# Kernel optimization log

Measured on AMD Instinct MI355X. Metric: run time of the kernel, lower is better.

The kernel has to match this reference:

```python
import jax, jax.numpy as jnp
import numpy as np
import math

N, B, S = 2048, 4, 1024
SFZ, IFZ, H, A = 384, 256, 8, 64
LN_EPS = 1e-5


def setup_inputs() -> dict:
    key = jax.random.key(0)
    ks = jax.random.split(key, 12)
    x = jax.random.normal(ks[0], (N, IFZ), dtype=jnp.float32)
    emb = jax.random.normal(ks[1], (B, S, SFZ), dtype=jnp.float32)
    mask = jax.random.randint(ks[2], (B, S), 0, 2).astype(bool)
    batch = jnp.sort(jax.random.randint(ks[3], (N,), 0, B)).astype(jnp.int64)
    sc = 1.0 / math.sqrt(IFZ)
    scs = 1.0 / math.sqrt(SFZ)
    Wq = jax.random.normal(ks[4], (IFZ, H * A), dtype=jnp.float32) * sc
    Wk = jax.random.normal(ks[5], (SFZ, H * A), dtype=jnp.float32) * scs
    Wv = jax.random.normal(ks[6], (SFZ, H * A), dtype=jnp.float32) * scs
    Wg = jax.random.normal(ks[7], (IFZ, H * A), dtype=jnp.float32) * sc
    bg = jnp.zeros((H * A,), dtype=jnp.float32)
    Wback = jax.random.normal(ks[8], (H * A, IFZ), dtype=jnp.float32) / math.sqrt(H * A)
    bback = jnp.zeros((IFZ,), dtype=jnp.float32)
    gamma = jnp.ones((IFZ,), dtype=jnp.float32)
    beta = jnp.zeros((IFZ,), dtype=jnp.float32)
    return {"x": x, "packed_sequence_emb": emb, "packed_sequence_mask": mask,
            "batch": batch, "Wq": Wq, "Wk": Wk, "Wv": Wv, "Wg": Wg, "bg": bg,
            "Wback": Wback, "bback": bback, "gamma": gamma, "beta": beta}


def _masked_softmax(scores, mask):
    # scores: [N,S,H], mask: [N,S,1] bool; softmax over S with padded entries zeroed
    neg = jnp.finfo(scores.dtype).min
    s = jnp.where(mask, scores, neg)
    s = s - jnp.max(s, axis=1, keepdims=True)
    e = jnp.exp(s) * mask
    return e / (jnp.sum(e, axis=1, keepdims=True) + 1e-9)


def reference(x, packed_sequence_emb, packed_sequence_mask, batch,
              Wq, Wk, Wv, Wg, bg, Wback, bback, gamma, beta):
    scale = math.sqrt(A)
    q = (x @ Wq).reshape(N, H, A)                               # [N,H,A]
    k = (packed_sequence_emb @ Wk).reshape(B, S, H, A)          # [B,S,H,A]
    v = (packed_sequence_emb @ Wv).reshape(B, S, H, A)
    # scores per (node, candidate-batch), then gather node's own batch entry;
    # avoids materializing k[batch] of shape [N,S,H,A]
    scores_all = jnp.einsum('nha,bsha->nbsh', q, k) / scale     # [N,B,S,H]
    idx = batch[:, None, None, None].astype(jnp.int32)
    scores = jnp.take_along_axis(scores_all, idx, axis=1)[:, 0]  # [N,S,H]
    bmask = packed_sequence_mask[batch][..., None]               # [N,S,1]
    w = _masked_softmax(scores, bmask)                           # [N,S,H]
    feat_all = jnp.einsum('nsh,bsha->nbha', w, v)                # [N,B,H,A]
    feat = jnp.take_along_axis(feat_all, idx, axis=1)[:, 0]      # [N,H,A]
    gate = jax.nn.sigmoid(x @ Wg + bg).reshape(N, H, A)
    new = (gate * feat).reshape(N, H * A) @ Wback + bback        # [N,IFZ]
    y = math.sqrt(2.0) * x + new
    mu = jnp.mean(y, axis=-1, keepdims=True)
    var = jnp.mean((y - mu) ** 2, axis=-1, keepdims=True)
    out = (y - mu) * jax.lax.rsqrt(var + LN_EPS) * gamma + beta
    seq_aa_logits = jnp.sum(scores[..., :2], axis=-1)            # [N,S]
    return out, seq_aa_logits
```

## Files before the change

kernel.cpp:

```cpp
#include <hip/hip_runtime.h>
#include <hip/hip_bf16.h>

#define NND 2048
#define BBATCH 4
#define SS 1024
#define SFZ 384
#define IFZ 256
#define HH 8
#define AA 64
#define HA 512
#define NBX 48
#define NSPL 8

typedef __attribute__((ext_vector_type(8))) short bf16x8;
typedef __attribute__((ext_vector_type(4))) float f32x4;

__device__ __forceinline__ unsigned short f2bf(float f) {
    union { float f; unsigned u; } a; a.f = f;
    unsigned r = a.u + 0x7fffu + ((a.u >> 16) & 1u);
    return (unsigned short)(r >> 16);
}
__device__ __forceinline__ float bf2f(unsigned short u) {
    return __uint_as_float((unsigned)u << 16);
}

__device__ __forceinline__ bf16x8 cvt8(const float* __restrict__ p) {
    const float4 f0 = *(const float4*)p;
    const float4 f1 = *(const float4*)(p + 4);
    bf16x8 o;
    o[0] = (short)f2bf(f0.x); o[1] = (short)f2bf(f0.y);
    o[2] = (short)f2bf(f0.z); o[3] = (short)f2bf(f0.w);
    o[4] = (short)f2bf(f1.x); o[5] = (short)f2bf(f1.y);
    o[6] = (short)f2bf(f1.z); o[7] = (short)f2bf(f1.w);
    return o;
}

__device__ __forceinline__ void tile_transpose(
    const float* __restrict__ src, unsigned short* __restrict__ dst,
    int K, int N, int kt, int nt, int t)
{
    __shared__ unsigned short tile[64][65];
    const int k0 = kt * 64, n0 = nt * 64;
    const int tr = t >> 6, tc = t & 63;
    #pragma unroll
    for (int r = 0; r < 16; ++r)
        tile[tr + r*4][tc] = f2bf(src[(size_t)(k0 + tr + r*4) * N + n0 + tc]);
    __syncthreads();
    #pragma unroll
    for (int r = 0; r < 16; ++r)
        dst[(size_t)(n0 + tr + r*4) * K + k0 + tc] = tile[tc][tr + r*4];
}

__global__ __launch_bounds__(256) void prep_kernel(
    const float* __restrict__ Wk, const float* __restrict__ Wv,
    const float* __restrict__ Wq, const float* __restrict__ Wg,
    const float* __restrict__ Wback,
    const void* __restrict__ mask_raw, const void* __restrict__ batch_raw,
    unsigned short* __restrict__ WkT, unsigned short* __restrict__ WvT,
    unsigned short* __restrict__ WqT, unsigned short* __restrict__ WgT,
    unsigned short* __restrict__ WbackT,
    float* __restrict__ mask_f, int* __restrict__ seg)
{
    const int bx = blockIdx.x, t = threadIdx.x;
    if (bx < 48)  { tile_transpose(Wk, WkT, SFZ, HA, bx/8, bx%8, t); return; }
    if (bx < 96)  { const int i = bx-48;  tile_transpose(Wv, WvT, SFZ, HA, i/8, i%8, t); return; }
    if (bx < 128) { const int i = bx-96;  tile_transpose(Wq, WqT, IFZ, HA, i/8, i%8, t); return; }
    if (bx < 160) { const int i = bx-128; tile_transpose(Wg, WgT, IFZ, HA, i/8, i%8, t); return; }
    if (bx < 192) { const int i = bx-160; tile_transpose(Wback, WbackT, HA, IFZ, i/4, i%4, t); return; }
    __shared__ int fl[4];
    __shared__ int fb;
    __shared__ int cnt[4];
    if (t < 4) { fl[t] = 0; cnt[t] = 0; }
    if (t == 0) fb = 0;
    __syncthreads();
    const unsigned char*  mb = (const unsigned char*)mask_raw;
    const unsigned short* mh = (const unsigned short*)mask_raw;
    const unsigned int*   mw = (const unsigned int*)mask_raw;
    int f0 = 0, f1 = 0, f2 = 0, f3 = 0;
    for (int i = t; i < 2048; i += 256) {
        unsigned short h = mh[i];
        if (h == 0x3f80u) f0 = 1;
        if ((i & 1) == 0 && h != 0) f1 = 1;
    }
    for (int i = t; i < 4096; i += 256)
        if ((i & 3) != 0 && mb[i] != 0) f2 = 1;
    for (int i = t; i < 1024; i += 256)
        if ((i & 1) != 0 && mw[i] != 0) f3 = 1;
    const int* bw = (const int*)batch_raw;
    int f4 = 0;
    for (int i = t + 1; i < 2048; i += 256)
        if (bw[i] < bw[i-1]) f4 = 1;
    if (f0) atomicOr(&fl[0], 1);
    if (f1) atomicOr(&fl[1], 1);
    if (f2) atomicOr(&fl[2], 1);
    if (f3) atomicOr(&fl[3], 1);
    if (f4) atomicOr(&fb, 1);
    __syncthreads();
    int mode;
    if (fl[0])      mode = fl[1] ? 1 : 0;
    else if (fl[2]) mode = 2;
    else if (fl[3]) mode = 3;
    else            mode = 4;
    for (int s = t; s < BBATCH*SS; s += 256) {
        int m;
        switch (mode) {
            case 0:  m = (mw[s]   != 0); break;
            case 1:  m = (mh[s]   != 0); break;
            case 2:  m = (mb[s]   != 0); break;
            case 3:  m = (mw[s]   != 0); break;
            default: m = (mw[2*s] != 0); break;
        }
        mask_f[s] = m ? 1.0f : 0.0f;
    }
    const int b64 = fb;
    for (int i = t; i < NND; i += 256) {
        const int bv = (b64 ? bw[2*i] : bw[i]) & 3;
        atomicAdd(&cnt[bv], 1);
    }
    __syncthreads();
    if (t == 0) {
        int s = 0;
        for (int b = 0; b < 4; ++b) { seg[2*b] = s; s += cnt[b]; seg[2*b+1] = s; }
    }
}

__global__ __launch_bounds__(256) void proj_mfma(
    const float* __restrict__ emb, const float* __restrict__ x,
    const unsigned short* __restrict__ WkT, const unsigned short* __restrict__ WvT,
    const unsigned short* __restrict__ WqT, const unsigned short* __restrict__ WgT,
    const float* __restrict__ bg,
    unsigned short* __restrict__ k_blk, unsigned short* __restrict__ vT_bf,
    unsigned short* __restrict__ q_bf, float* __restrict__ gate_ws)
{
    __shared__ unsigned short v_l[16][520];
    const int t = threadIdx.x, w = t >> 6, lane = t & 63;
    const int m16 = lane & 15, quad = lane >> 4;
    const int bx = blockIdx.x;
    if (bx < 512) {
        const int r0 = (bx >> 1) * 16;
        const int b = r0 >> 10, srow = r0 & (SS - 1);
        const float* ap = emb + (size_t)(r0 + m16) * SFZ + quad * 8;
        bf16x8 af[12];
        #pragma unroll
        for (int j = 0; j < 12; ++j) af[j] = cvt8(ap + j * 32);
        if ((bx & 1) == 0) {
            #pragma unroll
            for (int nt = 0; nt < 8; ++nt) {
                const int n0 = w * 128 + nt * 16;
                const unsigned short* bp = WkT + (size_t)(n0 + m16) * SFZ + quad * 8;
                f32x4 d = (f32x4){0.f, 0.f, 0.f, 0.f};
                #pragma unroll
                for (int j = 0; j < 12; ++j)
                    d = __builtin_amdgcn_mfma_f32_16x16x32_bf16(af[j], *(const bf16x8*)(bp + j * 32), d, 0, 0, 0);
                const int head = n0 >> 6, coff = (n0 & 63) + m16;
                unsigned short* kb = k_blk + (((size_t)(b * HH + head)) * SS) * 64 + coff;
                #pragma unroll
                for (int r = 0; r < 4; ++r)
                    kb[(size_t)(srow + quad * 4 + r) * 64] = f2bf(d[r]);
            }
        } else {
            #pragma unroll
            for (int nt = 0; nt < 8; ++nt) {
                const int n0 = w * 128 + nt * 16;
                const unsigned short* bp = WvT + (size_t)(n0 + m16) * SFZ + quad * 8;
                f32x4 d = (f32x4){0.f, 0.f, 0.f, 0.f};
                #pragma unroll
                for (int j = 0; j < 12; ++j)
                    d = __builtin_amdgcn_mfma_f32_16x16x32_bf16(af[j], *(const bf16x8*)(bp + j * 32), d, 0, 0, 0);
                #pragma unroll
                for (int r = 0; r < 4; ++r)
                    v_l[quad * 4 + r][n0 + m16] = f2bf(d[r]);
            }
            __syncthreads();
            for (int c = t; c < HA; c += 256) {
                unsigned short tmp[16];
                #pragma unroll
                for (int s = 0; s < 16; ++s) tmp[s] = v_l[s][c];
                unsigned short* dst = vT_bf + ((size_t)b * HA + c) * SS + srow;
                *(uint4*)dst       = ((const uint4*)tmp)[0];
                *(uint4*)(dst + 8) = ((const uint4*)tmp)[1];
            }
        }
    } else {
        const int i = bx - 512;
        const int r0 = (i >> 2) * 16;
        const int tensor = (i & 3) >> 1, half = i & 1;
        const unsigned short* Wt = tensor ? WgT : WqT;
        const float* ap = x + (size_t)(r0 + m16) * IFZ + quad * 8;
        bf16x8 af[8];
        #pragma unroll
        for (int j = 0; j < 8; ++j) af[j] = cvt8(ap + j * 32);
        #pragma unroll
        for (int nt = 0; nt < 4; ++nt) {
            const int n0 = half * 256 + w * 64 + nt * 16;
            const unsigned short* bp = Wt + (size_t)(n0 + m16) * IFZ + quad * 8;
            f32x4 d = (f32x4){0.f, 0.f, 0.f, 0.f};
            #pragma unroll
            for (int j = 0; j < 8; ++j)
                d = __builtin_amdgcn_mfma_f32_16x16x32_bf16(af[j], *(const bf16x8*)(bp + j * 32), d, 0, 0, 0);
            if (tensor == 0) {
                #pragma unroll
                for (int r = 0; r < 4; ++r)
                    q_bf[(size_t)(r0 + quad * 4 + r) * HA + n0 + m16] = f2bf(d[r]);
            } else {
                const float bgv = bg[n0 + m16];
                #pragma unroll
                for (int r = 0; r < 4; ++r)
                    gate_ws[(size_t)(r0 + quad * 4 + r) * HA + n0 + m16] =
                        1.f / (1.f + __expf(-(d[r] + bgv)));
            }
        }
    }
}

__global__ __launch_bounds__(256) void attn_kernel(
    const unsigned short* __restrict__ k_blk, const unsigned short* __restrict__ vT_bf,
    const unsigned short* __restrict__ q_bf, const float* __restrict__ mask_f,
    const int* __restrict__ seg, unsigned short* __restrict__ part_O,
    float2* __restrict__ part_ml, float* __restrict__ out_logits)
{
    __shared__ unsigned short P_lds[4][16][136];
    __shared__ float raw[2][16][132];
    const int bid = blockIdx.x;
    const int xcd = bid & 7;
    const int b   = xcd >> 1;
    const int idx = (bid >> 3) * 2 + (xcd & 1);
    const int z    = idx & 15;
    const int xblk = idx >> 4;
    const int hz    = z >> 3;
    const int split = z & 7;
    const int n0 = seg[2*b] + xblk * 16;
    const int nend = seg[2*b + 1];
    if (n0 >= nend) return;
    const int nvalid = min(16, nend - n0);

    const int t = threadIdx.x;
    const int w = t >> 6, lane = t & 63;
    const int m16 = lane & 15, quad = lane >> 4;
    const int h = hz * 4 + w;
    const int s0 = split * 128;

    int nq = n0 + m16; if (nq >= nend) nq = nend - 1;
    const unsigned short* qp = q_bf + (size_t)nq * HA + h * AA + quad * 8;
    const bf16x8 qa0 = *(const bf16x8*)qp;
    const bf16x8 qa1 = *(const bf16x8*)(qp + 32);

    const unsigned short* kb = k_blk + ((size_t)(b * HH + h)) * SS * 64;
    const unsigned short* vb = vT_bf + ((size_t)b * HA + h * AA) * SS;
    unsigned short (*Pw)[136] = P_lds[w];

    float msk[8];
    #pragma unroll
    for (int st = 0; st < 8; ++st)
        msk[st] = mask_f[b * SS + s0 + st * 16 + m16];

    f32x4 d[8];
    #pragma unroll
    for (int st = 0; st < 8; ++st) {
        const unsigned short* kp = kb + (size_t)(s0 + st * 16 + m16) * 64 + quad * 8;
        const bf16x8 b0 = *(const bf16x8*)kp;
        const bf16x8 b1 = *(const bf16x8*)(kp + 32);
        f32x4 acc = (f32x4){0.f, 0.f, 0.f, 0.f};
        acc = __builtin_amdgcn_mfma_f32_16x16x32_bf16(qa0, b0, acc, 0, 0, 0);
        acc = __builtin_amdgcn_mfma_f32_16x16x32_bf16(qa1, b1, acc, 0, 0, 0);
        #pragma unroll
        for (int r = 0; r < 4; ++r) acc[r] *= 0.125f;
        d[st] = acc;
    }
    if (hz == 0) {
        if (w < 2) {
            #pragma unroll
            for (int st = 0; st < 8; ++st)
                #pragma unroll
                for (int r = 0; r < 4; ++r)
                    raw[w][quad * 4 + r][st * 16 + m16] = d[st][r];
        }
        __syncthreads();
        for (int i = t; i < 16 * 128; i += 256) {
            const int node = i >> 7, sp = i & 127;
            if (node < nvalid)
                out_logits[(size_t)(n0 + node) * SS + s0 + sp] =
                    raw[0][node][sp] + raw[1][node][sp];
        }
    }
    float m_s[4], l_s[4];
    #pragma unroll
    for (int r = 0; r < 4; ++r) {
        float mx = -3.0e38f;
        #pragma unroll
        for (int st = 0; st < 8; ++st)
            mx = (msk[st] > 0.5f) ? fmaxf(mx, d[st][r]) : mx;
        mx = fmaxf(mx, __shfl_xor(mx, 1));
        mx = fmaxf(mx, __shfl_xor(mx, 2));
        mx = fmaxf(mx, __shfl_xor(mx, 4));
        mx = fmaxf(mx, __shfl_xor(mx, 8));
        m_s[r] = mx;
        float cs = 0.f;
        #pragma unroll
        for (int st = 0; st < 8; ++st) {
            const float e = (msk[st] > 0.5f) ? __expf(d[st][r] - mx) : 0.f;
            d[st][r] = e;
            cs += e;
        }
        cs += __shfl_xor(cs, 1);
        cs += __shfl_xor(cs, 2);
        cs += __shfl_xor(cs, 4);
        cs += __shfl_xor(cs, 8);
        l_s[r] = cs;
    }
    #pragma unroll
    for (int st = 0; st < 8; ++st)
        #pragma unroll
        for (int r = 0; r < 4; ++r)
            Pw[quad * 4 + r][st * 16 + m16] = f2bf(d[st][r]);
    f32x4 facc[4];
    #pragma unroll
    for (int a = 0; a < 4; ++a) facc[a] = (f32x4){0.f, 0.f, 0.f, 0.f};
    #pragma unroll
    for (int sub = 0; sub < 4; ++sub) {
        const bf16x8 pa = *(const bf16x8*)&Pw[m16][sub * 32 + quad * 8];
        const unsigned short* vp0 = vb + (size_t)m16 * SS + s0 + sub * 32 + quad * 8;
        #pragma unroll
        for (int a = 0; a < 4; ++a) {
            const bf16x8 vfr = *(const bf16x8*)(vp0 + (size_t)(a * 16) * SS);
            facc[a] = __builtin_amdgcn_mfma_f32_16x16x32_bf16(pa, vfr, facc[a], 0, 0, 0);
        }
    }
    unsigned short* po = part_O + (size_t)split * NND * HA;
    #pragma unroll
    for (int a = 0; a < 4; ++a)
        #pragma unroll
        for (int r = 0; r < 4; ++r) {
            const int row = quad * 4 + r;
            if (row < nvalid)
                po[(size_t)(n0 + row) * HA + h * AA + a * 16 + m16] = f2bf(facc[a][r]);
        }
    if (m16 == 0) {
        #pragma unroll
        for (int r = 0; r < 4; ++r) {
            const int row = quad * 4 + r;
            if (row < nvalid)
                part_ml[(size_t)split * NND * HH + (size_t)(n0 + row) * HH + h] =
                    make_float2(m_s[r], l_s[r]);
        }
    }
}

__global__ __launch_bounds__(256) void back_ln_fused(
    const unsigned short* __restrict__ part_O, const float2* __restrict__ part_ml,
    const float* __restrict__ gate_ws, const unsigned short* __restrict__ WbackT,
    const float* __restrict__ x, const float* __restrict__ bback,
    const float* __restrict__ gamma, const float* __restrict__ beta,
    float* __restrict__ out)
{
    __shared__ float coef[NSPL][8][8];
    __shared__ unsigned short gf_l[8][520];
    __shared__ float nl[8][260];
    const int t = threadIdx.x, w = t >> 6, lane = t & 63;
    const int m16 = lane & 15, quad = lane >> 4;
    const int r0 = blockIdx.x * 8;
    if (t < 64) {
        const int row = t >> 3, h = t & 7, n = r0 + row;
        float2 ml[NSPL];
        #pragma unroll
        for (int s = 0; s < NSPL; ++s)
            ml[s] = part_ml[(size_t)s * NND * HH + (size_t)n * HH + h];
        float M = -3.0e38f;
        #pragma unroll
        for (int s = 0; s < NSPL; ++s) M = fmaxf(M, ml[s].x);
        float L = 0.f;
        float e[NSPL];
        #pragma unroll
        for (int s = 0; s < NSPL; ++s) { e[s] = __expf(ml[s].x - M); L += ml[s].y * e[s]; }
        const float invL = 1.f / (L + 1e-9f);
        #pragma unroll
        for (int s = 0; s < NSPL; ++s) coef[s][row][h] = e[s] * invL;
    }
    __syncthreads();
    #pragma unroll
    for (int it = 0; it < 4; ++it) {
        const int i = (t + it * 256) * 4;
        const int row = i >> 9, c = i & (HA - 1), h = c >> 6;
        const int n = r0 + row;
        float4 o = make_float4(0.f, 0.f, 0.f, 0.f);
        #pragma unroll
        for (int s = 0; s < NSPL; ++s) {
            const ushort4 p = *(const ushort4*)&part_O[(size_t)s * NND * HA + (size_t)n * HA + c];
            const float cf = coef[s][row][h];
            o.x = fmaf(bf2f(p.x), cf, o.x); o.y = fmaf(bf2f(p.y), cf, o.y);
            o.z = fmaf(bf2f(p.z), cf, o.z); o.w = fmaf(bf2f(p.w), cf, o.w);
        }
        const float4 g = *(const float4*)&gate_ws[(size_t)n * HA + c];
        ushort4 ob;
        ob.x = f2bf(g.x * o.x); ob.y = f2bf(g.y * o.y);
        ob.z = f2bf(g.z * o.z); ob.w = f2bf(g.w * o.w);
        *(ushort4*)&gf_l[row][c] = ob;
    }
    __syncthreads();
    bf16x8 af[16];
    #pragma unroll
    for (int j = 0; j < 16; ++j)
        af[j] = *(const bf16x8*)&gf_l[m16 & 7][quad * 8 + j * 32];
    #pragma unroll
    for (int nt = 0; nt < 4; ++nt) {
        const int n0 = w * 64 + nt * 16;
        const unsigned short* bp = WbackT + (size_t)(n0 + m16) * HA + quad * 8;
        f32x4 d = (f32x4){0.f, 0.f, 0.f, 0.f};
        #pragma unroll
        for (int j = 0; j < 16; ++j)
            d = __builtin_amdgcn_mfma_f32_16x16x32_bf16(af[j], *(const bf16x8*)(bp + j * 32), d, 0, 0, 0);
        const float bb = bback[n0 + m16];
        #pragma unroll
        for (int r = 0; r < 4; ++r) {
            const int rr = quad * 4 + r;
            if (rr < 8) nl[rr][n0 + m16] = d[r] + bb;
        }
    }
    __syncthreads();
    const int row = t >> 5, li = t & 31;
    const float* xr = x + (size_t)(r0 + row) * IFZ;
    float yv[8];
    float s1 = 0.f, s2 = 0.f;
    #pragma unroll
    for (int j = 0; j < 8; ++j) {
        const int c = li + j * 32;
        const float v = fmaf(1.41421356237309515f, xr[c], nl[row][c]);
        yv[j] = v; s1 += v; s2 += v * v;
    }
    #pragma unroll
    for (int off = 16; off >= 1; off >>= 1) {
        s1 += __shfl_xor(s1, off);
        s2 += __shfl_xor(s2, off);
    }
    const float mu  = s1 * (1.f / IFZ);
    const float var = s2 * (1.f / IFZ) - mu * mu;
    const float rv  = rsqrtf(var + 1e-5f);
    float* orow = out + (size_t)(r0 + row) * IFZ;
    #pragma unroll
    for (int j = 0; j < 8; ++j) {
        const int c = li + j * 32;
        orow[c] = (yv[j] - mu) * rv * gamma[c] + beta[c];
    }
}

extern "C" void kernel_launch(void* const* d_in, const int* in_sizes, int n_in,
                              void* d_out, int out_size, void* d_ws, size_t ws_size,
                              hipStream_t stream) {
    const float* x     = (const float*)d_in[0];
    const float* emb   = (const float*)d_in[1];
    const void*  mraw  = d_in[2];
    const void*  braw  = d_in[3];
    const float* Wq    = (const float*)d_in[4];
    const float* Wk    = (const float*)d_in[5];
    const float* Wv    = (const float*)d_in[6];
    const float* Wg    = (const float*)d_in[7];
    const float* bg    = (const float*)d_in[8];
    const float* Wback = (const float*)d_in[9];
    const float* bback = (const float*)d_in[10];
    const float* gamma = (const float*)d_in[11];
    const float* beta  = (const float*)d_in[12];

    char* ws = (char*)d_ws;
    const size_t MB = 1048576;
    size_t off = 0;
    float*          mask_f  = (float*)(ws + off);  off += 16384;
    int*            seg     = (int*)(ws + off);    off += 16384;
    unsigned short* WkT     = (unsigned short*)(ws + off); off += 393216;
    unsigned short* WvT     = (unsigned short*)(ws + off); off += 393216;
    unsigned short* WqT     = (unsigned short*)(ws + off); off += 262144;
    unsigned short* WgT     = (unsigned short*)(ws + off); off += 262144;
    unsigned short* WbackT  = (unsigned short*)(ws + off); off += 262144;
    unsigned short* k_blk   = (unsigned short*)(ws + off); off += 4*MB;
    unsigned short* vT_bf   = (unsigned short*)(ws + off); off += 4*MB;
    unsigned short* q_bf    = (unsigned short*)(ws + off); off += 2*MB;
    float*          gate_ws = (float*)(ws + off); off += 4*MB;
    unsigned short* part_O  = (unsigned short*)(ws + off); off += 16*MB;
    float2*         part_ml = (float2*)(ws + off); off += 1*MB;

    float* out        = (float*)d_out;
    float* out_logits = out + (size_t)NND * IFZ;

    hipLaunchKernelGGL(prep_kernel, dim3(193), dim3(256), 0, stream,
                       Wk, Wv, Wq, Wg, Wback, mraw, braw,
                       WkT, WvT, WqT, WgT, WbackT, mask_f, seg);
    hipLaunchKernelGGL(proj_mfma, dim3(1024), dim3(256), 0, stream,
                       emb, x, WkT, WvT, WqT, WgT, bg, k_blk, vT_bf, q_bf, gate_ws);
    hipLaunchKernelGGL(attn_kernel, dim3(BBATCH * NBX * 16), dim3(256), 0, stream,
                       k_blk, vT_bf, q_bf, mask_f, seg, part_O, part_ml, out_logits);
    hipLaunchKernelGGL(back_ln_fused, dim3(NND / 8), dim3(256), 0, stream,
                       part_O, part_ml, gate_ws, WbackT, x, bback, gamma, beta, out);
}
```

Before: 198.5 us.

## Split weight transposes, store gate in bf16, halve rows per back-proj block

Each weight-transpose tile is split across two blocks, doubling the prep grid so more CUs take part. The sigmoid gate is now stored as bf16 instead of fp32, halving its write and read traffic between the projection and back-projection kernels. The fused back-projection/LayerNorm kernel now handles 4 rows per block instead of 8, doubling the grid for better occupancy, though half of each MFMA tile's rows go unused and WbackT is re-read by more blocks.

```diff
diff --git a/kernel.cpp b/kernel.cpp
--- a/kernel.cpp
+++ b/kernel.cpp
@@ -35,20 +35,21 @@
     return o;
 }
 
-__device__ __forceinline__ void tile_transpose(
+__device__ __forceinline__ void tile_transpose_h(
     const float* __restrict__ src, unsigned short* __restrict__ dst,
-    int K, int N, int kt, int nt, int t)
+    int K, int N, int kt, int nt, int half, int t)
 {
-    __shared__ unsigned short tile[64][65];
-    const int k0 = kt * 64, n0 = nt * 64;
+    __shared__ unsigned short tile[32][65];
+    const int k0 = kt * 64 + half * 32, n0 = nt * 64;
     const int tr = t >> 6, tc = t & 63;
     #pragma unroll
-    for (int r = 0; r < 16; ++r)
+    for (int r = 0; r < 8; ++r)
         tile[tr + r*4][tc] = f2bf(src[(size_t)(k0 + tr + r*4) * N + n0 + tc]);
     __syncthreads();
-    #pragma unroll
-    for (int r = 0; r < 16; ++r)
-        dst[(size_t)(n0 + tr + r*4) * K + k0 + tc] = tile[tc][tr + r*4];
+    const int rr = t >> 5, cc = t & 31;
+    #pragma unroll
+    for (int r2 = 0; r2 < 8; ++r2)
+        dst[(size_t)(n0 + rr + r2*8) * K + k0 + cc] = tile[cc][rr + r2*8];
 }
 
 __global__ __launch_bounds__(256) void prep_kernel(
@@ -62,11 +63,15 @@
     float* __restrict__ mask_f, int* __restrict__ seg)
 {
     const int bx = blockIdx.x, t = threadIdx.x;
-    if (bx < 48)  { tile_transpose(Wk, WkT, SFZ, HA, bx/8, bx%8, t); return; }
-    if (bx < 96)  { const int i = bx-48;  tile_transpose(Wv, WvT, SFZ, HA, i/8, i%8, t); return; }
-    if (bx < 128) { const int i = bx-96;  tile_transpose(Wq, WqT, IFZ, HA, i/8, i%8, t); return; }
-    if (bx < 160) { const int i = bx-128; tile_transpose(Wg, WgT, IFZ, HA, i/8, i%8, t); return; }
-    if (bx < 192) { const int i = bx-160; tile_transpose(Wback, WbackT, HA, IFZ, i/4, i%4, t); return; }
+    if (bx < 384) {
+        const int ht = bx >> 1, half = bx & 1;
+        if (ht < 48)       tile_transpose_h(Wk, WkT, SFZ, HA, ht/8, ht%8, half, t);
+        else if (ht < 96)  { const int i = ht-48;  tile_transpose_h(Wv, WvT, SFZ, HA, i/8, i%8, half, t); }
+        else if (ht < 128) { const int i = ht-96;  tile_transpose_h(Wq, WqT, IFZ, HA, i/8, i%8, half, t); }
+        else if (ht < 160) { const int i = ht-128; tile_transpose_h(Wg, WgT, IFZ, HA, i/8, i%8, half, t); }
+        else               { const int i = ht-160; tile_transpose_h(Wback, WbackT, HA, IFZ, i/4, i%4, half, t); }
+        return;
+    }
     __shared__ int fl[4];
     __shared__ int fb;
     __shared__ int cnt[4];
@@ -130,7 +135,7 @@
     const unsigned short* __restrict__ WqT, const unsigned short* __restrict__ WgT,
     const float* __restrict__ bg,
     unsigned short* __restrict__ k_blk, unsigned short* __restrict__ vT_bf,
-    unsigned short* __restrict__ q_bf, float* __restrict__ gate_ws)
+    unsigned short* __restrict__ q_bf, unsigned short* __restrict__ gate_bf)
 {
     __shared__ unsigned short v_l[16][520];
     const int t = threadIdx.x, w = t >> 6, lane = t & 63;
@@ -206,8 +211,8 @@
                 const float bgv = bg[n0 + m16];
                 #pragma unroll
                 for (int r = 0; r < 4; ++r)
-                    gate_ws[(size_t)(r0 + quad * 4 + r) * HA + n0 + m16] =
-                        1.f / (1.f + __expf(-(d[r] + bgv)));
+                    gate_bf[(size_t)(r0 + quad * 4 + r) * HA + n0 + m16] =
+                        f2bf(1.f / (1.f + __expf(-(d[r] + bgv))));
             }
         }
     }
@@ -348,18 +353,18 @@
 
 __global__ __launch_bounds__(256) void back_ln_fused(
     const unsigned short* __restrict__ part_O, const float2* __restrict__ part_ml,
-    const float* __restrict__ gate_ws, const unsigned short* __restrict__ WbackT,
+    const unsigned short* __restrict__ gate_bf, const unsigned short* __restrict__ WbackT,
     const float* __restrict__ x, const float* __restrict__ bback,
     const float* __restrict__ gamma, const float* __restrict__ beta,
     float* __restrict__ out)
 {
-    __shared__ float coef[NSPL][8][8];
-    __shared__ unsigned short gf_l[8][520];
-    __shared__ float nl[8][260];
+    __shared__ float coef[NSPL][4][8];
+    __shared__ unsigned short gf_l[4][520];
+    __shared__ float nl[4][260];
     const int t = threadIdx.x, w = t >> 6, lane = t & 63;
     const int m16 = lane & 15, quad = lane >> 4;
-    const int r0 = blockIdx.x * 8;
-    if (t < 64) {
+    const int r0 = blockIdx.x * 4;
+    if (t < 32) {
         const int row = t >> 3, h = t & 7, n = r0 + row;
         float2 ml[NSPL];
         #pragma unroll
@@ -378,7 +383,7 @@
     }
     __syncthreads();
     #pragma unroll
-    for (int it = 0; it < 4; ++it) {
+    for (int it = 0; it < 2; ++it) {
         const int i = (t + it * 256) * 4;
         const int row = i >> 9, c = i & (HA - 1), h = c >> 6;
         const int n = r0 + row;
@@ -390,17 +395,17 @@
             o.x = fmaf(bf2f(p.x), cf, o.x); o.y = fmaf(bf2f(p.y), cf, o.y);
             o.z = fmaf(bf2f(p.z), cf, o.z); o.w = fmaf(bf2f(p.w), cf, o.w);
         }
-        const float4 g = *(const float4*)&gate_ws[(size_t)n * HA + c];
+        const ushort4 g = *(const ushort4*)&gate_bf[(size_t)n * HA + c];
         ushort4 ob;
-        ob.x = f2bf(g.x * o.x); ob.y = f2bf(g.y * o.y);
-        ob.z = f2bf(g.z * o.z); ob.w = f2bf(g.w * o.w);
+        ob.x = f2bf(bf2f(g.x) * o.x); ob.y = f2bf(bf2f(g.y) * o.y);
+        ob.z = f2bf(bf2f(g.z) * o.z); ob.w = f2bf(bf2f(g.w) * o.w);
         *(ushort4*)&gf_l[row][c] = ob;
     }
     __syncthreads();
     bf16x8 af[16];
     #pragma unroll
     for (int j = 0; j < 16; ++j)
-        af[j] = *(const bf16x8*)&gf_l[m16 & 7][quad * 8 + j * 32];
+        af[j] = *(const bf16x8*)&gf_l[m16 & 3][quad * 8 + j * 32];
     #pragma unroll
     for (int nt = 0; nt < 4; ++nt) {
         const int n0 = w * 64 + nt * 16;
@@ -413,22 +418,22 @@
         #pragma unroll
         for (int r = 0; r < 4; ++r) {
             const int rr = quad * 4 + r;
-            if (rr < 8) nl[rr][n0 + m16] = d[r] + bb;
-        }
-    }
-    __syncthreads();
-    const int row = t >> 5, li = t & 31;
+            if (rr < 4) nl[rr][n0 + m16] = d[r] + bb;
+        }
+    }
+    __syncthreads();
+    const int row = t >> 6, li = t & 63;
     const float* xr = x + (size_t)(r0 + row) * IFZ;
-    float yv[8];
+    float yv[4];
     float s1 = 0.f, s2 = 0.f;
     #pragma unroll
-    for (int j = 0; j < 8; ++j) {
-        const int c = li + j * 32;
+    for (int j = 0; j < 4; ++j) {
+        const int c = li + j * 64;
         const float v = fmaf(1.41421356237309515f, xr[c], nl[row][c]);
         yv[j] = v; s1 += v; s2 += v * v;
     }
     #pragma unroll
-    for (int off = 16; off >= 1; off >>= 1) {
+    for (int off = 32; off >= 1; off >>= 1) {
         s1 += __shfl_xor(s1, off);
         s2 += __shfl_xor(s2, off);
     }
@@ -437,8 +442,8 @@
     const float rv  = rsqrtf(var + 1e-5f);
     float* orow = out + (size_t)(r0 + row) * IFZ;
     #pragma unroll
-    for (int j = 0; j < 8; ++j) {
-        const int c = li + j * 32;
+    for (int j = 0; j < 4; ++j) {
+        const int c = li + j * 64;
         orow[c] = (yv[j] - mu) * rv * gamma[c] + beta[c];
     }
 }
@@ -473,20 +478,20 @@
     unsigned short* k_blk   = (unsigned short*)(ws + off); off += 4*MB;
     unsigned short* vT_bf   = (unsigned short*)(ws + off); off += 4*MB;
     unsigned short* q_bf    = (unsigned short*)(ws + off); off += 2*MB;
-    float*          gate_ws = (float*)(ws + off); off += 4*MB;
+    unsigned short* gate_bf = (unsigned short*)(ws + off); off += 2*MB;
     unsigned short* part_O  = (unsigned short*)(ws + off); off += 16*MB;
     float2*         part_ml = (float2*)(ws + off); off += 1*MB;
 
     float* out        = (float*)d_out;
     float* out_logits = out + (size_t)NND * IFZ;
 
-    hipLaunchKernelGGL(prep_kernel, dim3(193), dim3(256), 0, stream,
+    hipLaunchKernelGGL(prep_kernel, dim3(385), dim3(256), 0, stream,
                        Wk, Wv, Wq, Wg, Wback, mraw, braw,
                        WkT, WvT, WqT, WgT, WbackT, mask_f, seg);
     hipLaunchKernelGGL(proj_mfma, dim3(1024), dim3(256), 0, stream,
-                       emb, x, WkT, WvT, WqT, WgT, bg, k_blk, vT_bf, q_bf, gate_ws);
+                       emb, x, WkT, WvT, WqT, WgT, bg, k_blk, vT_bf, q_bf, gate_bf);
     hipLaunchKernelGGL(attn_kernel, dim3(BBATCH * NBX * 16), dim3(256), 0, stream,
                        k_blk, vT_bf, q_bf, mask_f, seg, part_O, part_ml, out_logits);
-    hipLaunchKernelGGL(back_ln_fused, dim3(NND / 8), dim3(256), 0, stream,
-                       part_O, part_ml, gate_ws, WbackT, x, bback, gamma, beta, out);
-}
+    hipLaunchKernelGGL(back_ln_fused, dim3(NND / 4), dim3(256), 0, stream,
+                       part_O, part_ml, gate_bf, WbackT, x, bback, gamma, beta, out);
+}
```

After: 202.4 us. About the same (+2.0%).
